# Performance work log

Hardware: AMD Instinct MI355X
Metric: run time of the kernel (lower is better)

## Reference

```python
import jax, jax.numpy as jnp
import numpy as np

NX, NQ, NU, NY = 256, 64, 8, 4
N = 65536
EPS = 0.01
STD = 0.5


def setup_inputs() -> dict:
    key = jax.random.key(0)
    ks = jax.random.split(key, 8)
    return {
        "x": jax.random.normal(ks[0], (N, NX), jnp.float32),
        "u": jax.random.normal(ks[1], (N, NU), jnp.float32),
        "X": jax.random.normal(ks[2], (NX + NQ, NX + NQ), jnp.float32) * STD,
        "U": jax.random.normal(ks[3], (NX, NQ), jnp.float32) * STD,
        "Y1": jax.random.normal(ks[4], (NX, NX), jnp.float32) * STD,
        "XP": jax.random.normal(ks[5], (NX, NX), jnp.float32) * STD,
        "B2": jax.random.normal(ks[6], (NX, NU), jnp.float32) * STD,
        "D12": jax.random.normal(ks[7], (NQ, NU), jnp.float32) * STD,
        "bv": jnp.zeros((NQ,), jnp.float32),
        "t": 0,
    }


def _constrained(X, U, Y1, XP):
    # updateParameters(): build A, B1, C1, D11 from unconstrained params.
    P = XP @ XP.T + EPS * jnp.eye(NX, dtype=XP.dtype)
    H = X @ X.T + EPS * jnp.eye(NX + NQ, dtype=X.dtype)
    H11, H12, H22 = H[:NX, :NX], H[:NX, NX:], H[NX:, NX:]
    Y = -0.5 * (H11 + Y1 - Y1.T)
    Pinv = jnp.linalg.inv(P)
    A = Pinv @ Y                                   # [nx, nx]
    lam = 0.5 * jnp.diagonal(H22)                  # Lambda diagonal
    D11 = -jnp.tril(H22, -1) / lam[:, None]        # strictly lower triangular [nq, nq]
    C1 = U.T / lam[:, None]                        # [nq, nx]
    B1 = Pinv @ (-H12 - U)                         # [nx, nq]
    return A, B1, C1, D11


def _calc_w(base, D11):
    # Forward substitution: w_i = relu(base_i + sum_{j<i} D11[i,j] * w_j).
    # D11 is strictly lower triangular and unfilled w columns are zero, so a
    # full matvec against the carry is exact.
    nq = base.shape[1]

    def step(w, inp):
        i, row, b_col = inp                        # row: [nq], b_col: [Nbatch]
        wi = jax.nn.relu(b_col + w @ row)
        return w.at[:, i].set(wi), None

    w0 = jnp.zeros_like(base)
    w, _ = jax.lax.scan(step, w0, (jnp.arange(nq), D11, base.T))
    return w


def reference(x, u, X, U, Y1, XP, B2, D12, bv, t):
    A, B1, C1, D11 = _constrained(X, U, Y1, XP)
    base = x @ C1.T + u @ D12.T + bv               # [N, nq]
    w = _calc_w(base, D11)
    x_dot = x @ A.T + w @ B1.T + u @ B2.T          # [N, nx]
    return x_dot
```

## Files before the change

kernel.cpp:

```cpp
#include <hip/hip_runtime.h>

#define EPS_C 0.01f

typedef __attribute__((ext_vector_type(8))) short short8;
typedef __attribute__((ext_vector_type(4))) float f32x4;
typedef __attribute__((ext_vector_type(4))) unsigned short u16x4;
typedef __attribute__((ext_vector_type(8))) unsigned short u16x8;

#define WS_H    0
#define WS_C    102400
#define WS_C2   167936
#define WS_Y    233472
#define WS_RHS  299008
#define WS_D11  331776
#define WS_WFH  419840
#define WS_WFM  464896
#define WS_WFL  509952
#define WS_BBH  555008
#define WS_BBM  564224
#define WS_BBL  573440
#define WS_WG   582656
#define WS_E0   4776960
#define WS_E1   4781056

__device__ __forceinline__ int wfoff(int n, int k) {
    return (((n >> 4) * 44 + (k >> 5) * 4 + ((k >> 3) & 3)) << 7) + ((n & 15) << 3) + (k & 7);
}
__device__ __forceinline__ int bboff(int n, int k) {
    return (((n >> 4) * 36 + (k >> 5) * 4 + ((k >> 3) & 3)) << 7) + ((n & 15) << 3) + (k & 7);
}

__device__ __forceinline__ unsigned short f2bf(float f) {
    unsigned int u = __float_as_uint(f);
    unsigned int r = (u + 0x7fffu + ((u >> 16) & 1u)) >> 16;
    return (unsigned short)r;
}
__device__ __forceinline__ float bf2f(unsigned short h) {
    return __uint_as_float(((unsigned int)h) << 16);
}
__device__ __forceinline__ void split1(float f, unsigned short& h, unsigned short& m, unsigned short& l) {
    h = f2bf(f);
    float r1 = f - bf2f(h);
    m = f2bf(r1);
    l = f2bf(r1 - bf2f(m));
}
__device__ __forceinline__ void split8(const float* v, short8& h8, short8& m8, short8& l8) {
#pragma unroll
    for (int j = 0; j < 8; ++j) {
        unsigned short h, m, l;
        split1(v[j], h, m, l);
        h8[j] = (short)h; m8[j] = (short)m; l8[j] = (short)l;
    }
}

__global__ void k_build(const float* __restrict__ Xm, const float* __restrict__ XPm,
                        float* __restrict__ H, float* __restrict__ P) {
    int idx = blockIdx.x * 256 + threadIdx.x;
    if (idx < 102400) {
        int i = idx / 320, j = idx - i * 320;
        const float4* a = (const float4*)(Xm + i * 320);
        const float4* b = (const float4*)(Xm + j * 320);
        float s = 0.f;
        for (int k = 0; k < 80; ++k) {
            float4 va = a[k], vb = b[k];
            s += va.x * vb.x + va.y * vb.y + va.z * vb.z + va.w * vb.w;
        }
        H[idx] = (i == j) ? s + EPS_C : s;
    } else {
        idx -= 102400;
        if (idx < 65536) {
            int i = idx >> 8, j = idx & 255;
            const float4* a = (const float4*)(XPm + i * 256);
            const float4* b = (const float4*)(XPm + j * 256);
            float s = 0.f;
            for (int k = 0; k < 64; ++k) {
                float4 va = a[k], vb = b[k];
                s += va.x * vb.x + va.y * vb.y + va.z * vb.z + va.w * vb.w;
            }
            P[idx] = (i == j) ? s + EPS_C : s;
        }
    }
}

__global__ void k_derived(const float* __restrict__ H, const float* __restrict__ Um,
                          const float* __restrict__ Y1, const float* __restrict__ B2,
                          const float* __restrict__ D12,
                          float* __restrict__ Y, float* __restrict__ RHS,
                          float* __restrict__ D11g,
                          unsigned short* __restrict__ Bh, unsigned short* __restrict__ Bm,
                          unsigned short* __restrict__ Bl,
                          unsigned short* __restrict__ Bbh, unsigned short* __restrict__ Bbm,
                          unsigned short* __restrict__ Bbl) {
    int idx = blockIdx.x * 256 + threadIdx.x;
    if (idx < 65536) {
        int i = idx >> 8, j = idx & 255;
        Y[idx] = -0.5f * (H[i * 320 + j] + Y1[i * 256 + j] - Y1[j * 256 + i]);
        return;
    }
    idx -= 65536;
    if (idx < 16384) {
        RHS[idx] = -H[(idx >> 6) * 320 + 256 + (idx & 63)] - Um[idx];
        return;
    }
    idx -= 16384;
    if (idx < 4096) {
        int q = idx >> 6, j = idx & 63;
        float lam = 0.5f * H[(256 + q) * 320 + 256 + q];
        D11g[idx] = (j < q) ? -H[(256 + q) * 320 + 256 + j] / lam : 0.f;
        return;
    }
    idx -= 4096;
    if (idx < 8192) {
        int o = idx >> 5, cc = idx & 31;
        float f = (cc < 8) ? B2[o * 8 + cc] : 0.f;
        unsigned short h, m, l;
        split1(f, h, m, l);
        int off = wfoff(o, 256 + cc);
        Bh[off] = h; Bm[off] = m; Bl[off] = l;
        return;
    }
    idx -= 8192;
    if (idx < 18432) {
        int q = idx / 288, k = idx - q * 288;
        float f;
        if (k < 256) {
            float lam = 0.5f * H[(256 + q) * 320 + 256 + q];
            f = Um[(size_t)k * 64 + q] / lam;
        } else if (k < 264) f = D12[(size_t)q * 8 + (k - 256)];
        else f = 0.f;
        unsigned short h, m, l;
        split1(f, h, m, l);
        int off = bboff(q, k);
        Bbh[off] = h; Bbm[off] = m; Bbl[off] = l;
    }
}

__global__ void __launch_bounds__(256) k_inv8(const float* __restrict__ Cold, float* __restrict__ E, int b) {
    __shared__ __align__(16) float M[64 * 68];
    __shared__ __align__(16) float Rs[8 * 68];
    __shared__ __align__(16) float Ts[64 * 8];
    __shared__ float E8s[8 * 9];
    const int tid = threadIdx.x;
    const int ti = tid & 15, tj = tid >> 4;
#pragma unroll
    for (int t = 0; t < 4; ++t) {
        int e = tid + t * 256;
        int r = e >> 4, c4 = e & 15;
        float4 v = *(const float4*)&Cold[(size_t)(b * 64 + r) * 256 + b * 64 + c4 * 4];
        *(float4*)&M[r * 68 + c4 * 4] = v;
    }
    __syncthreads();
    for (int s = 0; s < 8; ++s) {
        if (tid < 64) {
            const int lane = tid;
            float e8[8];
#pragma unroll
            for (int j = 0; j < 8; ++j) e8[j] = 0.f;
            if (lane < 8) {
#pragma unroll
                for (int j = 0; j < 8; ++j) e8[j] = M[(s * 8 + lane) * 68 + s * 8 + j];
            }
#pragma unroll
            for (int k = 0; k < 8; ++k) {
                const float p = __shfl(e8[k], k);
                const float rinv = 1.0f / p;
                const float f = -e8[k] * rinv;
                const bool isk = (lane == k);
#pragma unroll
                for (int j = 0; j < 8; ++j) {
                    const float prj = __shfl(e8[j], k);
                    if (j == k) e8[j] = isk ? rinv : f;
                    else        e8[j] = isk ? prj * rinv : fmaf(f, prj, e8[j]);
                }
            }
            if (lane < 8) {
#pragma unroll
                for (int j = 0; j < 8; ++j) E8s[lane * 9 + j] = e8[j];
            }
        }
        __syncthreads();
#pragma unroll
        for (int t = 0; t < 2; ++t) {
            int e = tid + t * 256;
            int r = e >> 6, c = e & 63;
            Rs[r * 68 + c] = M[(s * 8 + r) * 68 + c];
        }
#pragma unroll
        for (int t = 0; t < 2; ++t) {
            int e = tid + t * 256;
            int i = e >> 3, c = e & 7;
            float acc = 0.f;
#pragma unroll
            for (int j = 0; j < 8; ++j) acc = fmaf(M[i * 68 + s * 8 + j], E8s[j * 9 + c], acc);
            Ts[i * 8 + c] = acc;
        }
        __syncthreads();
        {
            const bool rowIn = ((ti >> 1) == s);
            const bool colIn = ((tj >> 1) == s);
            const int i0 = ti * 4, j0 = tj * 4;
            float nv[4][4];
            if (rowIn && colIn) {
#pragma unroll
                for (int r = 0; r < 4; ++r)
#pragma unroll
                    for (int d = 0; d < 4; ++d)
                        nv[r][d] = E8s[(i0 - s * 8 + r) * 9 + (j0 - s * 8 + d)];
            } else if (rowIn) {
#pragma unroll
                for (int r = 0; r < 4; ++r)
#pragma unroll
                    for (int d = 0; d < 4; ++d) {
                        float acc = 0.f;
#pragma unroll
                        for (int c = 0; c < 8; ++c)
                            acc = fmaf(E8s[(i0 - s * 8 + r) * 9 + c], Rs[c * 68 + j0 + d], acc);
                        nv[r][d] = acc;
                    }
            } else if (colIn) {
#pragma unroll
                for (int r = 0; r < 4; ++r)
#pragma unroll
                    for (int d = 0; d < 4; ++d)
                        nv[r][d] = -Ts[(i0 + r) * 8 + (j0 - s * 8 + d)];
            } else {
#pragma unroll
                for (int r = 0; r < 4; ++r)
#pragma unroll
                    for (int d = 0; d < 4; ++d) {
                        float acc = M[(i0 + r) * 68 + j0 + d];
#pragma unroll
                        for (int c = 0; c < 8; ++c)
                            acc = fmaf(-Ts[(i0 + r) * 8 + c], Rs[c * 68 + j0 + d], acc);
                        nv[r][d] = acc;
                    }
            }
#pragma unroll
            for (int r = 0; r < 4; ++r)
#pragma unroll
                for (int d = 0; d < 4; ++d) M[(i0 + r) * 68 + j0 + d] = nv[r][d];
        }
        __syncthreads();
    }
#pragma unroll
    for (int t = 0; t < 4; ++t) {
        int e = tid + t * 256;
        int r = e >> 4, c4 = e & 15;
        float4 v = *(const float4*)&M[r * 68 + c4 * 4];
        *(float4*)&E[(size_t)r * 64 + c4 * 4] = v;
    }
}

__global__ void __launch_bounds__(256) k_gjS(const float* __restrict__ Cold, float* __restrict__ Cnew,
                                             const float* __restrict__ E, float* __restrict__ Eout,
                                             int b, int nb) {
    const int I = blockIdx.x >> 2, J = blockIdx.x & 3;
    const int tid = threadIdx.x;
    const int ti = tid & 15, tj = tid >> 4;
    if (I == b && J == b) {
        const int r = tid >> 2, seg = tid & 3;
#pragma unroll
        for (int t = 0; t < 4; ++t) {
            float4 v = *(const float4*)&E[(size_t)r * 64 + seg * 16 + t * 4];
            *(float4*)&Cnew[(size_t)(b * 64 + r) * 256 + b * 64 + seg * 16 + t * 4] = v;
        }
        return;
    }
    __shared__ __align__(16) float Es[64 * 68];
    __shared__ __align__(16) float S1[64 * 68];
    __shared__ __align__(16) float S2[64 * 68];
    for (int e = tid; e < 1024; e += 256) {
        int r = e >> 4, c4 = e & 15;
        float4 v = *(const float4*)&E[(size_t)r * 64 + c4 * 4];
        *(float4*)&Es[r * 68 + c4 * 4] = v;
    }
    if (I == b) {
        for (int e = tid; e < 1024; e += 256) {
            int r = e >> 4, c4 = e & 15;
            float4 v = *(const float4*)&Cold[(size_t)(b * 64 + r) * 256 + J * 64 + c4 * 4];
            *(float4*)&S1[r * 68 + c4 * 4] = v;
        }
        __syncthreads();
        float acc[4][4];
#pragma unroll
        for (int r = 0; r < 4; ++r)
#pragma unroll
            for (int d = 0; d < 4; ++d) acc[r][d] = 0.f;
        for (int mm = 0; mm < 64; ++mm) {
            float a4[4], b4[4];
#pragma unroll
            for (int d = 0; d < 4; ++d) { a4[d] = Es[(ti * 4 + d) * 68 + mm]; b4[d] = S1[mm * 68 + tj * 4 + d]; }
#pragma unroll
            for (int r = 0; r < 4; ++r)
#pragma unroll
                for (int d = 0; d < 4; ++d) acc[r][d] = fmaf(a4[r], b4[d], acc[r][d]);
        }
#pragma unroll
        for (int r = 0; r < 4; ++r) {
            float4 v = {acc[r][0], acc[r][1], acc[r][2], acc[r][3]};
            *(float4*)&Cnew[(size_t)(b * 64 + ti * 4 + r) * 256 + J * 64 + tj * 4] = v;
        }
        return;
    }
    if (J == b) {
        for (int e = tid; e < 1024; e += 256) {
            int r = e >> 4, c4 = e & 15;
            float4 v = *(const float4*)&Cold[(size_t)(I * 64 + r) * 256 + b * 64 + c4 * 4];
            *(float4*)&S1[r * 68 + c4 * 4] = v;
        }
        __syncthreads();
        float acc[4][4];
#pragma unroll
        for (int r = 0; r < 4; ++r)
#pragma unroll
            for (int d = 0; d < 4; ++d) acc[r][d] = 0.f;
        for (int kk = 0; kk < 64; ++kk) {
            float a4[4], b4[4];
#pragma unroll
            for (int d = 0; d < 4; ++d) { a4[d] = S1[(ti * 4 + d) * 68 + kk]; b4[d] = Es[kk * 68 + tj * 4 + d]; }
#pragma unroll
            for (int r = 0; r < 4; ++r)
#pragma unroll
                for (int d = 0; d < 4; ++d) acc[r][d] = fmaf(a4[r], b4[d], acc[r][d]);
        }
#pragma unroll
        for (int r = 0; r < 4; ++r) {
            float4 v = {-acc[r][0], -acc[r][1], -acc[r][2], -acc[r][3]};
            *(float4*)&Cnew[(size_t)(I * 64 + ti * 4 + r) * 256 + b * 64 + tj * 4] = v;
        }
        return;
    }
    for (int e = tid; e < 1024; e += 256) {
        int r = e >> 4, c4 = e & 15;
        float4 v = *(const float4*)&Cold[(size_t)(I * 64 + r) * 256 + b * 64 + c4 * 4];
        *(float4*)&S1[r * 68 + c4 * 4] = v;
        float4 w = *(const float4*)&Cold[(size_t)(b * 64 + r) * 256 + J * 64 + c4 * 4];
        *(float4*)&S2[r * 68 + c4 * 4] = w;
    }
    __syncthreads();
    float t4[4][4];
#pragma unroll
    for (int r = 0; r < 4; ++r)
#pragma unroll
        for (int d = 0; d < 4; ++d) t4[r][d] = 0.f;
    for (int kk = 0; kk < 64; ++kk) {
        float a4[4], b4[4];
#pragma unroll
        for (int d = 0; d < 4; ++d) { a4[d] = S1[(ti * 4 + d) * 68 + kk]; b4[d] = Es[kk * 68 + tj * 4 + d]; }
#pragma unroll
        for (int r = 0; r < 4; ++r)
#pragma unroll
            for (int d = 0; d < 4; ++d) t4[r][d] = fmaf(a4[r], b4[d], t4[r][d]);
    }
    __syncthreads();
#pragma unroll
    for (int r = 0; r < 4; ++r)
#pragma unroll
        for (int d = 0; d < 4; ++d) S1[(ti * 4 + r) * 68 + tj * 4 + d] = t4[r][d];
    __syncthreads();
    float acc[4][4];
#pragma unroll
    for (int r = 0; r < 4; ++r) {
        float4 cv = *(const float4*)&Cold[(size_t)(I * 64 + ti * 4 + r) * 256 + J * 64 + tj * 4];
        acc[r][0] = cv.x; acc[r][1] = cv.y; acc[r][2] = cv.z; acc[r][3] = cv.w;
    }
    for (int kk = 0; kk < 64; ++kk) {
        float a4[4], b4[4];
#pragma unroll
        for (int d = 0; d < 4; ++d) { a4[d] = S1[(ti * 4 + d) * 68 + kk]; b4[d] = S2[kk * 68 + tj * 4 + d]; }
#pragma unroll
        for (int r = 0; r < 4; ++r)
#pragma unroll
            for (int d = 0; d < 4; ++d) acc[r][d] = fmaf(-a4[r], b4[d], acc[r][d]);
    }
#pragma unroll
    for (int r = 0; r < 4; ++r) {
        float4 v = {acc[r][0], acc[r][1], acc[r][2], acc[r][3]};
        *(float4*)&Cnew[(size_t)(I * 64 + ti * 4 + r) * 256 + J * 64 + tj * 4] = v;
    }
    if (I == nb && J == nb) {
        float* M   = Es;
        float* Rs2 = S2;
        float* Ts2 = S2 + 1024;
        float* E8s = S2 + 1664;
        __syncthreads();
#pragma unroll
        for (int r = 0; r < 4; ++r)
#pragma unroll
            for (int d = 0; d < 4; ++d)
                M[(ti * 4 + r) * 68 + tj * 4 + d] = acc[r][d];
        __syncthreads();
        for (int s = 0; s < 8; ++s) {
            if (tid < 64) {
                const int lane = tid;
                float e8[8];
#pragma unroll
                for (int j = 0; j < 8; ++j) e8[j] = 0.f;
                if (lane < 8) {
#pragma unroll
                    for (int j = 0; j < 8; ++j) e8[j] = M[(s * 8 + lane) * 68 + s * 8 + j];
                }
#pragma unroll
                for (int k = 0; k < 8; ++k) {
                    const float p = __shfl(e8[k], k);
                    const float rinv = 1.0f / p;
                    const float f = -e8[k] * rinv;
                    const bool isk = (lane == k);
#pragma unroll
                    for (int j = 0; j < 8; ++j) {
                        const float prj = __shfl(e8[j], k);
                        if (j == k) e8[j] = isk ? rinv : f;
                        else        e8[j] = isk ? prj * rinv : fmaf(f, prj, e8[j]);
                    }
                }
                if (lane < 8) {
#pragma unroll
                    for (int j = 0; j < 8; ++j) E8s[lane * 9 + j] = e8[j];
                }
            }
            __syncthreads();
#pragma unroll
            for (int t = 0; t < 2; ++t) {
                int e = tid + t * 256;
                int r = e >> 6, c = e & 63;
                Rs2[r * 68 + c] = M[(s * 8 + r) * 68 + c];
            }
#pragma unroll
            for (int t = 0; t < 2; ++t) {
                int e = tid + t * 256;
                int i = e >> 3, c = e & 7;
                float a2 = 0.f;
#pragma unroll
                for (int j = 0; j < 8; ++j) a2 = fmaf(M[i * 68 + s * 8 + j], E8s[j * 9 + c], a2);
                Ts2[i * 8 + c] = a2;
            }
            __syncthreads();
            {
                const bool rowIn = ((ti >> 1) == s);
                const bool colIn = ((tj >> 1) == s);
                const int i0 = ti * 4, j0 = tj * 4;
                float nv[4][4];
                if (rowIn && colIn) {
#pragma unroll
                    for (int r = 0; r < 4; ++r)
#pragma unroll
                        for (int d = 0; d < 4; ++d)
                            nv[r][d] = E8s[(i0 - s * 8 + r) * 9 + (j0 - s * 8 + d)];
                } else if (rowIn) {
#pragma unroll
                    for (int r = 0; r < 4; ++r)
#pragma unroll
                        for (int d = 0; d < 4; ++d) {
                            float a2 = 0.f;
#pragma unroll
                            for (int c = 0; c < 8; ++c)
                                a2 = fmaf(E8s[(i0 - s * 8 + r) * 9 + c], Rs2[c * 68 + j0 + d], a2);
                            nv[r][d] = a2;
                        }
                } else if (colIn) {
#pragma unroll
                    for (int r = 0; r < 4; ++r)
#pragma unroll
                        for (int d = 0; d < 4; ++d)
                            nv[r][d] = -Ts2[(i0 + r) * 8 + (j0 - s * 8 + d)];
                } else {
#pragma unroll
                    for (int r = 0; r < 4; ++r)
#pragma unroll
                        for (int d = 0; d < 4; ++d) {
                            float a2 = M[(i0 + r) * 68 + j0 + d];
#pragma unroll
                            for (int c = 0; c < 8; ++c)
                                a2 = fmaf(-Ts2[(i0 + r) * 8 + c], Rs2[c * 68 + j0 + d], a2);
                            nv[r][d] = a2;
                        }
                }
#pragma unroll
                for (int r = 0; r < 4; ++r)
#pragma unroll
                    for (int d = 0; d < 4; ++d) M[(i0 + r) * 68 + j0 + d] = nv[r][d];
            }
            __syncthreads();
        }
#pragma unroll
        for (int t = 0; t < 4; ++t) {
            int e = tid + t * 256;
            int r = e >> 4, c4 = e & 15;
            float4 v = *(const float4*)&M[r * 68 + c4 * 4];
            *(float4*)&Eout[(size_t)r * 64 + c4 * 4] = v;
        }
    }
}

__global__ void __launch_bounds__(256) k_apply2(const float* __restrict__ PI, const float* __restrict__ Y,
                                                const float* __restrict__ RHS,
                                                unsigned short* __restrict__ Bh, unsigned short* __restrict__ Bm,
                                                unsigned short* __restrict__ Bl) {
    const int i0 = ((int)blockIdx.x / 5) * 64;
    const int c0 = ((int)blockIdx.x % 5) * 64;
    __shared__ __align__(16) float S1[64 * 68], S2[64 * 68];
    const int tid = threadIdx.x;
    const int ti = tid & 15, tj = tid >> 4;
    float acc[4][4];
#pragma unroll
    for (int r = 0; r < 4; ++r)
#pragma unroll
        for (int d = 0; d < 4; ++d) acc[r][d] = 0.f;
    for (int kc = 0; kc < 4; ++kc) {
        __syncthreads();
        for (int e = tid; e < 1024; e += 256) {
            int i = e >> 4, k4 = e & 15;
            float4 v = *(const float4*)&PI[(size_t)(i0 + i) * 256 + kc * 64 + k4 * 4];
            S1[(k4 * 4 + 0) * 68 + i] = v.x;
            S1[(k4 * 4 + 1) * 68 + i] = v.y;
            S1[(k4 * 4 + 2) * 68 + i] = v.z;
            S1[(k4 * 4 + 3) * 68 + i] = v.w;
            float4 w;
            if (c0 < 256) w = *(const float4*)&Y[(size_t)(kc * 64 + i) * 256 + c0 + k4 * 4];
            else          w = *(const float4*)&RHS[(size_t)(kc * 64 + i) * 64 + k4 * 4];
            *(float4*)&S2[i * 68 + k4 * 4] = w;
        }
        __syncthreads();
        for (int kk = 0; kk < 64; ++kk) {
            float4 pv = *(const float4*)&S1[kk * 68 + ti * 4];
            float4 gv = *(const float4*)&S2[kk * 68 + tj * 4];
            float p4[4] = {pv.x, pv.y, pv.z, pv.w};
            float g4[4] = {gv.x, gv.y, gv.z, gv.w};
#pragma unroll
            for (int r = 0; r < 4; ++r)
#pragma unroll
                for (int d = 0; d < 4; ++d) acc[r][d] = fmaf(p4[r], g4[d], acc[r][d]);
        }
    }
    const int pc0 = (c0 < 256) ? c0 : 288;
#pragma unroll
    for (int r = 0; r < 4; ++r)
#pragma unroll
        for (int d = 0; d < 4; ++d) {
            unsigned short h, m, l;
            split1(acc[r][d], h, m, l);
            int off = wfoff(i0 + ti * 4 + r, pc0 + tj * 4 + d);
            Bh[off] = h; Bm[off] = m; Bl[off] = l;
        }
}

#define XSTR 264
__global__ void __launch_bounds__(256, 3) k_base(const float* __restrict__ x, const float* __restrict__ u,
                                                 const unsigned short* __restrict__ Bbh,
                                                 const unsigned short* __restrict__ Bbm,
                                                 const unsigned short* __restrict__ Bbl,
                                                 const float* __restrict__ bv,
                                                 float* __restrict__ wg) {
    __shared__ __align__(16) unsigned short Ah[32 * XSTR];
    __shared__ __align__(16) unsigned short Am[32 * XSTR];
    __shared__ __align__(16) unsigned short Al[32 * XSTR];
    const int tid = threadIdx.x;
    const int r0 = blockIdx.x * 32;
    {
        const float4* xg4 = (const float4*)(x + (size_t)r0 * 256);
#pragma unroll
        for (int i = 0; i < 8; ++i) {
            int e = tid + i * 256, r = e >> 6, c4 = e & 63;
            float4 v = xg4[e];
            float vv[4] = {v.x, v.y, v.z, v.w};
            u16x4 hv, mv, lv;
#pragma unroll
            for (int j = 0; j < 4; ++j) {
                unsigned short h, m, l;
                split1(vv[j], h, m, l);
                hv[j] = h; mv[j] = m; lv[j] = l;
            }
            *(u16x4*)&Ah[r * XSTR + c4 * 4] = hv;
            *(u16x4*)&Am[r * XSTR + c4 * 4] = mv;
            *(u16x4*)&Al[r * XSTR + c4 * 4] = lv;
        }
    }
    __syncthreads();
    const int lane = tid & 63, wid = tid >> 6;
    const int n0 = wid * 16;
    const int lr = lane & 15, lg = lane >> 4;
    const int lk = lg * 8;
    const int fb = wid * 4608 + lg * 128 + lr * 8;
    f32x4 acc[2];
    acc[0] = (f32x4){0.f, 0.f, 0.f, 0.f};
    acc[1] = (f32x4){0.f, 0.f, 0.f, 0.f};
    for (int kt = 0; kt < 9; ++kt) {
        const int ka = kt * 32 + lk;
        short8 a_h[2], a_m[2], a_l[2];
        if (kt < 8) {
            a_h[0] = *(const short8*)&Ah[lr * XSTR + ka];
            a_h[1] = *(const short8*)&Ah[(16 + lr) * XSTR + ka];
            a_m[0] = *(const short8*)&Am[lr * XSTR + ka];
            a_m[1] = *(const short8*)&Am[(16 + lr) * XSTR + ka];
            a_l[0] = *(const short8*)&Al[lr * XSTR + ka];
            a_l[1] = *(const short8*)&Al[(16 + lr) * XSTR + ka];
        } else {
            if (lg == 0) {
                float vv[8];
                const float4* up = (const float4*)&u[(size_t)(r0 + lr) * 8];
                float4 v0 = up[0], v1 = up[1];
                vv[0] = v0.x; vv[1] = v0.y; vv[2] = v0.z; vv[3] = v0.w;
                vv[4] = v1.x; vv[5] = v1.y; vv[6] = v1.z; vv[7] = v1.w;
                split8(vv, a_h[0], a_m[0], a_l[0]);
                const float4* up2 = (const float4*)&u[(size_t)(r0 + 16 + lr) * 8];
                float4 w0 = up2[0], w1 = up2[1];
                vv[0] = w0.x; vv[1] = w0.y; vv[2] = w0.z; vv[3] = w0.w;
                vv[4] = w1.x; vv[5] = w1.y; vv[6] = w1.z; vv[7] = w1.w;
                split8(vv, a_h[1], a_m[1], a_l[1]);
            } else {
                short8 z = {0, 0, 0, 0, 0, 0, 0, 0};
                a_h[0] = z; a_h[1] = z; a_m[0] = z; a_m[1] = z; a_l[0] = z; a_l[1] = z;
            }
        }
        const int off = fb + kt * 512;
        short8 b_h = *(const short8*)&Bbh[off];
        short8 b_m = *(const short8*)&Bbm[off];
        short8 b_l = *(const short8*)&Bbl[off];
#pragma unroll
        for (int m = 0; m < 2; ++m) {
            acc[m] = __builtin_amdgcn_mfma_f32_16x16x32_bf16(a_h[m], b_h, acc[m], 0, 0, 0);
            acc[m] = __builtin_amdgcn_mfma_f32_16x16x32_bf16(a_m[m], b_h, acc[m], 0, 0, 0);
            acc[m] = __builtin_amdgcn_mfma_f32_16x16x32_bf16(a_h[m], b_m, acc[m], 0, 0, 0);
            acc[m] = __builtin_amdgcn_mfma_f32_16x16x32_bf16(a_l[m], b_h, acc[m], 0, 0, 0);
            acc[m] = __builtin_amdgcn_mfma_f32_16x16x32_bf16(a_m[m], b_m, acc[m], 0, 0, 0);
            acc[m] = __builtin_amdgcn_mfma_f32_16x16x32_bf16(a_h[m], b_l, acc[m], 0, 0, 0);
        }
    }
    const float bvv = bv[n0 + lr];
#pragma unroll
    for (int m = 0; m < 2; ++m)
#pragma unroll
        for (int j = 0; j < 4; ++j)
            wg[(size_t)(r0 + m * 16 + lg * 4 + j) * 64 + n0 + lr] = acc[m][j] + bvv;
}

__global__ void __launch_bounds__(256) k_rec(float* __restrict__ wg, const float* __restrict__ D11g) {
    __shared__ float D[64 * 64];
    const int tid = threadIdx.x;
#pragma unroll
    for (int t = 0; t < 16; ++t) D[tid + t * 256] = D11g[tid + t * 256];
    __syncthreads();
    const size_t r = (size_t)blockIdx.x * 256 + tid;
    float w[64];
    float* wr = wg + r * 64;
#pragma unroll
    for (int c = 0; c < 16; ++c) {
        float4 v = *(const float4*)&wr[c * 4];
        w[4 * c] = v.x; w[4 * c + 1] = v.y; w[4 * c + 2] = v.z; w[4 * c + 3] = v.w;
    }
    w[0] = fmaxf(w[0], 0.f);
#pragma unroll
    for (int i = 1; i < 64; ++i) {
        float s0 = w[i], s1 = 0.f, s2 = 0.f, s3 = 0.f;
#pragma unroll
        for (int j = 0; j + 3 < i; j += 4) {
            s0 = fmaf(w[j + 0], D[i * 64 + j + 0], s0);
            s1 = fmaf(w[j + 1], D[i * 64 + j + 1], s1);
            s2 = fmaf(w[j + 2], D[i * 64 + j + 2], s2);
            s3 = fmaf(w[j + 3], D[i * 64 + j + 3], s3);
        }
#pragma unroll
        for (int j = i & ~3; j < i; ++j) s0 = fmaf(w[j], D[i * 64 + j], s0);
        w[i] = fmaxf((s0 + s1) + (s2 + s3), 0.f);
    }
#pragma unroll
    for (int c = 0; c < 16; ++c) {
        float4 v = {w[4 * c], w[4 * c + 1], w[4 * c + 2], w[4 * c + 3]};
        *(float4*)&wr[c * 4] = v;
    }
}

__global__ void __launch_bounds__(256, 3) k_m2(const float* __restrict__ x, const float* __restrict__ wg,
                                               const float* __restrict__ u,
                                               const unsigned short* __restrict__ Bh,
                                               const unsigned short* __restrict__ Bm,
                                               const unsigned short* __restrict__ Bl,
                                               float* __restrict__ out) {
    __shared__ __align__(16) unsigned short Ah[32 * XSTR];
    __shared__ __align__(16) unsigned short Am[32 * XSTR];
    __shared__ __align__(16) unsigned short Al[32 * XSTR];
    const int tid = threadIdx.x;
    const int r0 = blockIdx.x * 32;
    {
        const float4* xg4 = (const float4*)(x + (size_t)r0 * 256);
#pragma unroll
        for (int i = 0; i < 8; ++i) {
            int e = tid + i * 256, r = e >> 6, c4 = e & 63;
            float4 v = xg4[e];
            float vv[4] = {v.x, v.y, v.z, v.w};
            u16x4 hv, mv, lv;
#pragma unroll
            for (int j = 0; j < 4; ++j) {
                unsigned short h, m, l;
                split1(vv[j], h, m, l);
                hv[j] = h; mv[j] = m; lv[j] = l;
            }
            *(u16x4*)&Ah[r * XSTR + c4 * 4] = hv;
            *(u16x4*)&Am[r * XSTR + c4 * 4] = mv;
            *(u16x4*)&Al[r * XSTR + c4 * 4] = lv;
        }
    }
    __syncthreads();
    const int lane = tid & 63, wid = tid >> 6;
    const int n0 = wid * 64;
    const int lr = lane & 15, lg = lane >> 4;
    const int lk = lg * 8;
    const int lgoff = lg * 128 + lr * 8;
    int fb[4];
#pragma unroll
    for (int nf = 0; nf < 4; ++nf) fb[nf] = (wid * 4 + nf) * 5632 + lgoff;
    f32x4 acc[2][4];
#pragma unroll
    for (int m = 0; m < 2; ++m)
#pragma unroll
        for (int nf = 0; nf < 4; ++nf) acc[m][nf] = (f32x4){0.f, 0.f, 0.f, 0.f};

#define M2_MFMA6()                                                                               \
    for (int nf = 0; nf < 4; ++nf) {                                                             \
        for (int m = 0; m < 2; ++m) {                                                            \
            acc[m][nf] = __builtin_amdgcn_mfma_f32_16x16x32_bf16(a_h[m], b_h[nf], acc[m][nf], 0, 0, 0); \
            acc[m][nf] = __builtin_amdgcn_mfma_f32_16x16x32_bf16(a_m[m], b_h[nf], acc[m][nf], 0, 0, 0); \
            acc[m][nf] = __builtin_amdgcn_mfma_f32_16x16x32_bf16(a_h[m], b_m[nf], acc[m][nf], 0, 0, 0); \
            acc[m][nf] = __builtin_amdgcn_mfma_f32_16x16x32_bf16(a_l[m], b_h[nf], acc[m][nf], 0, 0, 0); \
            acc[m][nf] = __builtin_amdgcn_mfma_f32_16x16x32_bf16(a_m[m], b_m[nf], acc[m][nf], 0, 0, 0); \
            acc[m][nf] = __builtin_amdgcn_mfma_f32_16x16x32_bf16(a_h[m], b_l[nf], acc[m][nf], 0, 0, 0); \
        }                                                                                        \
    }

    for (int kt = 0; kt < 8; ++kt) {
        const int ka = kt * 32 + lk;
        short8 a_h[2], a_m[2], a_l[2];
        a_h[0] = *(const short8*)&Ah[lr * XSTR + ka];
        a_h[1] = *(const short8*)&Ah[(16 + lr) * XSTR + ka];
        a_m[0] = *(const short8*)&Am[lr * XSTR + ka];
        a_m[1] = *(const short8*)&Am[(16 + lr) * XSTR + ka];
        a_l[0] = *(const short8*)&Al[lr * XSTR + ka];
        a_l[1] = *(const short8*)&Al[(16 + lr) * XSTR + ka];
        short8 b_h[4], b_m[4], b_l[4];
#pragma unroll
        for (int nf = 0; nf < 4; ++nf) {
            const int off = fb[nf] + kt * 512;
            b_h[nf] = *(const short8*)&Bh[off];
            b_m[nf] = *(const short8*)&Bm[off];
            b_l[nf] = *(const short8*)&Bl[off];
        }
#pragma unroll
        M2_MFMA6()
    }
    {
        short8 a_h[2], a_m[2], a_l[2];
        if (lg == 0) {
            float vv[8];
            const float4* up = (const float4*)&u[(size_t)(r0 + lr) * 8];
            float4 v0 = up[0], v1 = up[1];
            vv[0] = v0.x; vv[1] = v0.y; vv[2] = v0.z; vv[3] = v0.w;
            vv[4] = v1.x; vv[5] = v1.y; vv[6] = v1.z; vv[7] = v1.w;
            split8(vv, a_h[0], a_m[0], a_l[0]);
            const float4* up2 = (const float4*)&u[(size_t)(r0 + 16 + lr) * 8];
            float4 w0 = up2[0], w1 = up2[1];
            vv[0] = w0.x; vv[1] = w0.y; vv[2] = w0.z; vv[3] = w0.w;
            vv[4] = w1.x; vv[5] = w1.y; vv[6] = w1.z; vv[7] = w1.w;
            split8(vv, a_h[1], a_m[1], a_l[1]);
        } else {
            short8 z = {0, 0, 0, 0, 0, 0, 0, 0};
            a_h[0] = z; a_h[1] = z; a_m[0] = z; a_m[1] = z; a_l[0] = z; a_l[1] = z;
        }
        short8 b_h[4], b_m[4], b_l[4];
#pragma unroll
        for (int nf = 0; nf < 4; ++nf) {
            const int off = fb[nf] + 8 * 512;
            b_h[nf] = *(const short8*)&Bh[off];
            b_m[nf] = *(const short8*)&Bm[off];
            b_l[nf] = *(const short8*)&Bl[off];
        }
#pragma unroll
        M2_MFMA6()
    }
    for (int kt = 9; kt < 11; ++kt) {
        const int wc = (kt - 9) * 32 + lk;
        short8 a_h[2], a_m[2], a_l[2];
        {
            float vv[8];
            const float4* wp = (const float4*)&wg[(size_t)(r0 + lr) * 64 + wc];
            float4 v0 = wp[0], v1 = wp[1];
            vv[0] = v0.x; vv[1] = v0.y; vv[2] = v0.z; vv[3] = v0.w;
            vv[4] = v1.x; vv[5] = v1.y; vv[6] = v1.z; vv[7] = v1.w;
            split8(vv, a_h[0], a_m[0], a_l[0]);
            const float4* wp2 = (const float4*)&wg[(size_t)(r0 + 16 + lr) * 64 + wc];
            float4 w0 = wp2[0], w1 = wp2[1];
            vv[0] = w0.x; vv[1] = w0.y; vv[2] = w0.z; vv[3] = w0.w;
            vv[4] = w1.x; vv[5] = w1.y; vv[6] = w1.z; vv[7] = w1.w;
            split8(vv, a_h[1], a_m[1], a_l[1]);
        }
        short8 b_h[4], b_m[4], b_l[4];
#pragma unroll
        for (int nf = 0; nf < 4; ++nf) {
            const int off = fb[nf] + kt * 512;
            b_h[nf] = *(const short8*)&Bh[off];
            b_m[nf] = *(const short8*)&Bm[off];
            b_l[nf] = *(const short8*)&Bl[off];
        }
#pragma unroll
        for (int nf = 0; nf < 4; ++nf) {
#pragma unroll
            for (int m = 0; m < 2; ++m) {
                acc[m][nf] = __builtin_amdgcn_mfma_f32_16x16x32_bf16(a_h[m], b_h[nf], acc[m][nf], 0, 0, 0);
                acc[m][nf] = __builtin_amdgcn_mfma_f32_16x16x32_bf16(a_m[m], b_h[nf], acc[m][nf], 0, 0, 0);
                acc[m][nf] = __builtin_amdgcn_mfma_f32_16x16x32_bf16(a_h[m], b_m[nf], acc[m][nf], 0, 0, 0);
                acc[m][nf] = __builtin_amdgcn_mfma_f32_16x16x32_bf16(a_l[m], b_h[nf], acc[m][nf], 0, 0, 0);
                acc[m][nf] = __builtin_amdgcn_mfma_f32_16x16x32_bf16(a_m[m], b_m[nf], acc[m][nf], 0, 0, 0);
                acc[m][nf] = __builtin_amdgcn_mfma_f32_16x16x32_bf16(a_h[m], b_l[nf], acc[m][nf], 0, 0, 0);
                acc[m][nf] = __builtin_amdgcn_mfma_f32_16x16x32_bf16(a_m[m], b_l[nf], acc[m][nf], 0, 0, 0);
                acc[m][nf] = __builtin_amdgcn_mfma_f32_16x16x32_bf16(a_l[m], b_m[nf], acc[m][nf], 0, 0, 0);
            }
        }
    }
#pragma unroll
    for (int m = 0; m < 2; ++m)
#pragma unroll
        for (int nf = 0; nf < 4; ++nf)
#pragma unroll
            for (int j = 0; j < 4; ++j)
                out[(size_t)(r0 + m * 16 + lg * 4 + j) * 256 + n0 + nf * 16 + lr] = acc[m][nf][j];
}

extern "C" void kernel_launch(void* const* d_in, const int* in_sizes, int n_in,
                              void* d_out, int out_size, void* d_ws, size_t ws_size,
                              hipStream_t stream) {
    const float* x   = (const float*)d_in[0];
    const float* u   = (const float*)d_in[1];
    const float* Xm  = (const float*)d_in[2];
    const float* Um  = (const float*)d_in[3];
    const float* Y1  = (const float*)d_in[4];
    const float* XPm = (const float*)d_in[5];
    const float* B2  = (const float*)d_in[6];
    const float* D12 = (const float*)d_in[7];
    const float* bv  = (const float*)d_in[8];
    float* out = (float*)d_out;
    float* ws  = (float*)d_ws;

    float* H    = ws + WS_H;
    float* C0   = ws + WS_C;
    float* C1   = ws + WS_C2;
    float* Y    = ws + WS_Y;
    float* RHS  = ws + WS_RHS;
    float* D11g = ws + WS_D11;
    float* E0   = ws + WS_E0;
    float* E1   = ws + WS_E1;
    unsigned short* Bh  = (unsigned short*)(ws + WS_WFH);
    unsigned short* Bm  = (unsigned short*)(ws + WS_WFM);
    unsigned short* Bl  = (unsigned short*)(ws + WS_WFL);
    unsigned short* Bbh = (unsigned short*)(ws + WS_BBH);
    unsigned short* Bbm = (unsigned short*)(ws + WS_BBM);
    unsigned short* Bbl = (unsigned short*)(ws + WS_BBL);
    float* wg = ws + WS_WG;

    k_build<<<656, 256, 0, stream>>>(Xm, XPm, H, C0);
    k_derived<<<441, 256, 0, stream>>>(H, Um, Y1, B2, D12, Y, RHS, D11g,
                                       Bh, Bm, Bl, Bbh, Bbm, Bbl);
    k_base<<<2048, 256, 0, stream>>>(x, u, Bbh, Bbm, Bbl, bv, wg);
    k_rec<<<256, 256, 0, stream>>>(wg, D11g);
    k_inv8<<<1, 256, 0, stream>>>(C0, E0, 0);
    k_gjS<<<16, 256, 0, stream>>>(C0, C1, E0, E1, 0, 1);
    k_gjS<<<16, 256, 0, stream>>>(C1, C0, E1, E0, 1, 2);
    k_gjS<<<16, 256, 0, stream>>>(C0, C1, E0, E1, 2, 3);
    k_gjS<<<16, 256, 0, stream>>>(C1, C0, E1, E0, 3, -1);
    k_apply2<<<20, 256, 0, stream>>>(C0, Y, RHS, Bh, Bm, Bl);
    k_m2<<<2048, 256, 0, stream>>>(x, wg, u, Bh, Bm, Bl, out);
}
```

Measured before the change: 340.7 us.

## Fuse matrix inversion stages with grid barrier and merge base with recurrence

Moves the first diagonal-block inverse into an extra block of the derived-parameter kernel. All Gauss-Jordan block steps plus the apply step now run in one persistent kernel that synchronises through an atomic-counter grid barrier, replacing six small launches. The base GEMM and the forward-substitution recurrence are also fused, so w no longer makes a round trip through global memory. The cost is that only 32 threads per block run the recurrence, occupancy drops to 2 blocks per CU, and the spin barrier relies on all 20 blocks being resident at once.

```diff
diff --git a/kernel.cpp b/kernel.cpp
--- a/kernel.cpp
+++ b/kernel.cpp
@@ -22,6 +22,7 @@
 #define WS_WG   582656
 #define WS_E0   4776960
 #define WS_E1   4781056
+#define WS_CTR  4785152
 
 __device__ __forceinline__ int wfoff(int n, int k) {
     return (((n >> 4) * 44 + (k >> 5) * 4 + ((k >> 3) & 3)) << 7) + ((n & 15) << 3) + (k & 7);
@@ -51,6 +52,17 @@
         split1(v[j], h, m, l);
         h8[j] = (short)h; m8[j] = (short)m; l8[j] = (short)l;
     }
+}
+
+__device__ __forceinline__ void gbar(unsigned int* ctr, unsigned int tgt) {
+    __syncthreads();
+    if (threadIdx.x == 0) {
+        __threadfence();
+        atomicAdd(ctr, 1u);
+        while (atomicAdd(ctr, 0u) < tgt) { __builtin_amdgcn_s_sleep(8); }
+        __threadfence();
+    }
+    __syncthreads();
 }
 
 __global__ void k_build(const float* __restrict__ Xm, const float* __restrict__ XPm,
@@ -82,7 +94,7 @@
     }
 }
 
-__global__ void k_derived(const float* __restrict__ H, const float* __restrict__ Um,
+__global__ void __launch_bounds__(256) k_derived(const float* __restrict__ H, const float* __restrict__ Um,
                           const float* __restrict__ Y1, const float* __restrict__ B2,
                           const float* __restrict__ D12,
                           float* __restrict__ Y, float* __restrict__ RHS,
@@ -90,8 +102,126 @@
                           unsigned short* __restrict__ Bh, unsigned short* __restrict__ Bm,
                           unsigned short* __restrict__ Bl,
                           unsigned short* __restrict__ Bbh, unsigned short* __restrict__ Bbm,
-                          unsigned short* __restrict__ Bbl) {
-    int idx = blockIdx.x * 256 + threadIdx.x;
+                          unsigned short* __restrict__ Bbl,
+                          const float* __restrict__ C0, float* __restrict__ E0,
+                          unsigned int* __restrict__ ctr) {
+    __shared__ __align__(16) float M[64 * 68];
+    __shared__ __align__(16) float Rs[8 * 68];
+    __shared__ __align__(16) float Ts[64 * 8];
+    __shared__ float E8s[8 * 9];
+    const int tid = threadIdx.x;
+    if (blockIdx.x == 441) {
+        const int ti = tid & 15, tj = tid >> 4;
+#pragma unroll
+        for (int t = 0; t < 4; ++t) {
+            int e = tid + t * 256;
+            int r = e >> 4, c4 = e & 15;
+            float4 v = *(const float4*)&C0[(size_t)r * 256 + c4 * 4];
+            *(float4*)&M[r * 68 + c4 * 4] = v;
+        }
+        __syncthreads();
+        for (int s = 0; s < 8; ++s) {
+            if (tid < 64) {
+                const int lane = tid;
+                float e8[8];
+#pragma unroll
+                for (int j = 0; j < 8; ++j) e8[j] = 0.f;
+                if (lane < 8) {
+#pragma unroll
+                    for (int j = 0; j < 8; ++j) e8[j] = M[(s * 8 + lane) * 68 + s * 8 + j];
+                }
+#pragma unroll
+                for (int k = 0; k < 8; ++k) {
+                    const float p = __shfl(e8[k], k);
+                    const float rinv = 1.0f / p;
+                    const float f = -e8[k] * rinv;
+                    const bool isk = (lane == k);
+#pragma unroll
+                    for (int j = 0; j < 8; ++j) {
+                        const float prj = __shfl(e8[j], k);
+                        if (j == k) e8[j] = isk ? rinv : f;
+                        else        e8[j] = isk ? prj * rinv : fmaf(f, prj, e8[j]);
+                    }
+                }
+                if (lane < 8) {
+#pragma unroll
+                    for (int j = 0; j < 8; ++j) E8s[lane * 9 + j] = e8[j];
+                }
+            }
+            __syncthreads();
+#pragma unroll
+            for (int t = 0; t < 2; ++t) {
+                int e = tid + t * 256;
+                int r = e >> 6, c = e & 63;
+                Rs[r * 68 + c] = M[(s * 8 + r) * 68 + c];
+            }
+#pragma unroll
+            for (int t = 0; t < 2; ++t) {
+                int e = tid + t * 256;
+                int i = e >> 3, c = e & 7;
+                float acc = 0.f;
+#pragma unroll
+                for (int j = 0; j < 8; ++j) acc = fmaf(M[i * 68 + s * 8 + j], E8s[j * 9 + c], acc);
+                Ts[i * 8 + c] = acc;
+            }
+            __syncthreads();
+            {
+                const bool rowIn = ((ti >> 1) == s);
+                const bool colIn = ((tj >> 1) == s);
+                const int i0 = ti * 4, j0 = tj * 4;
+                float nv[4][4];
+                if (rowIn && colIn) {
+#pragma unroll
+                    for (int r = 0; r < 4; ++r)
+#pragma unroll
+                        for (int d = 0; d < 4; ++d)
+                            nv[r][d] = E8s[(i0 - s * 8 + r) * 9 + (j0 - s * 8 + d)];
+                } else if (rowIn) {
+#pragma unroll
+                    for (int r = 0; r < 4; ++r)
+#pragma unroll
+                        for (int d = 0; d < 4; ++d) {
+                            float acc = 0.f;
+#pragma unroll
+                            for (int c = 0; c < 8; ++c)
+                                acc = fmaf(E8s[(i0 - s * 8 + r) * 9 + c], Rs[c * 68 + j0 + d], acc);
+                            nv[r][d] = acc;
+                        }
+                } else if (colIn) {
+#pragma unroll
+                    for (int r = 0; r < 4; ++r)
+#pragma unroll
+                        for (int d = 0; d < 4; ++d)
+                            nv[r][d] = -Ts[(i0 + r) * 8 + (j0 - s * 8 + d)];
+                } else {
+#pragma unroll
+                    for (int r = 0; r < 4; ++r)
+#pragma unroll
+                        for (int d = 0; d < 4; ++d) {
+                            float acc = M[(i0 + r) * 68 + j0 + d];
+#pragma unroll
+                            for (int c = 0; c < 8; ++c)
+                                acc = fmaf(-Ts[(i0 + r) * 8 + c], Rs[c * 68 + j0 + d], acc);
+                            nv[r][d] = acc;
+                        }
+                }
+#pragma unroll
+                for (int r = 0; r < 4; ++r)
+#pragma unroll
+                    for (int d = 0; d < 4; ++d) M[(i0 + r) * 68 + j0 + d] = nv[r][d];
+            }
+            __syncthreads();
+        }
+#pragma unroll
+        for (int t = 0; t < 4; ++t) {
+            int e = tid + t * 256;
+            int r = e >> 4, c4 = e & 15;
+            float4 v = *(const float4*)&M[r * 68 + c4 * 4];
+            *(float4*)&E0[(size_t)r * 64 + c4 * 4] = v;
+        }
+        return;
+    }
+    int idx = blockIdx.x * 256 + tid;
     if (idx < 65536) {
         int i = idx >> 8, j = idx & 255;
         Y[idx] = -0.5f * (H[i * 320 + j] + Y1[i * 256 + j] - Y1[j * 256 + i]);
@@ -132,428 +262,326 @@
         split1(f, h, m, l);
         int off = bboff(q, k);
         Bbh[off] = h; Bbm[off] = m; Bbl[off] = l;
-    }
-}
-
-__global__ void __launch_bounds__(256) k_inv8(const float* __restrict__ Cold, float* __restrict__ E, int b) {
-    __shared__ __align__(16) float M[64 * 68];
-    __shared__ __align__(16) float Rs[8 * 68];
-    __shared__ __align__(16) float Ts[64 * 8];
-    __shared__ float E8s[8 * 9];
-    const int tid = threadIdx.x;
-    const int ti = tid & 15, tj = tid >> 4;
-#pragma unroll
-    for (int t = 0; t < 4; ++t) {
-        int e = tid + t * 256;
-        int r = e >> 4, c4 = e & 15;
-        float4 v = *(const float4*)&Cold[(size_t)(b * 64 + r) * 256 + b * 64 + c4 * 4];
-        *(float4*)&M[r * 68 + c4 * 4] = v;
-    }
-    __syncthreads();
-    for (int s = 0; s < 8; ++s) {
-        if (tid < 64) {
-            const int lane = tid;
-            float e8[8];
-#pragma unroll
-            for (int j = 0; j < 8; ++j) e8[j] = 0.f;
-            if (lane < 8) {
-#pragma unroll
-                for (int j = 0; j < 8; ++j) e8[j] = M[(s * 8 + lane) * 68 + s * 8 + j];
-            }
-#pragma unroll
-            for (int k = 0; k < 8; ++k) {
-                const float p = __shfl(e8[k], k);
-                const float rinv = 1.0f / p;
-                const float f = -e8[k] * rinv;
-                const bool isk = (lane == k);
-#pragma unroll
-                for (int j = 0; j < 8; ++j) {
-                    const float prj = __shfl(e8[j], k);
-                    if (j == k) e8[j] = isk ? rinv : f;
-                    else        e8[j] = isk ? prj * rinv : fmaf(f, prj, e8[j]);
-                }
-            }
-            if (lane < 8) {
-#pragma unroll
-                for (int j = 0; j < 8; ++j) E8s[lane * 9 + j] = e8[j];
-            }
-        }
-        __syncthreads();
-#pragma unroll
-        for (int t = 0; t < 2; ++t) {
-            int e = tid + t * 256;
-            int r = e >> 6, c = e & 63;
-            Rs[r * 68 + c] = M[(s * 8 + r) * 68 + c];
-        }
-#pragma unroll
-        for (int t = 0; t < 2; ++t) {
-            int e = tid + t * 256;
-            int i = e >> 3, c = e & 7;
-            float acc = 0.f;
-#pragma unroll
-            for (int j = 0; j < 8; ++j) acc = fmaf(M[i * 68 + s * 8 + j], E8s[j * 9 + c], acc);
-            Ts[i * 8 + c] = acc;
-        }
-        __syncthreads();
-        {
-            const bool rowIn = ((ti >> 1) == s);
-            const bool colIn = ((tj >> 1) == s);
-            const int i0 = ti * 4, j0 = tj * 4;
-            float nv[4][4];
-            if (rowIn && colIn) {
-#pragma unroll
-                for (int r = 0; r < 4; ++r)
-#pragma unroll
-                    for (int d = 0; d < 4; ++d)
-                        nv[r][d] = E8s[(i0 - s * 8 + r) * 9 + (j0 - s * 8 + d)];
-            } else if (rowIn) {
-#pragma unroll
-                for (int r = 0; r < 4; ++r)
-#pragma unroll
-                    for (int d = 0; d < 4; ++d) {
-                        float acc = 0.f;
-#pragma unroll
-                        for (int c = 0; c < 8; ++c)
-                            acc = fmaf(E8s[(i0 - s * 8 + r) * 9 + c], Rs[c * 68 + j0 + d], acc);
-                        nv[r][d] = acc;
-                    }
-            } else if (colIn) {
-#pragma unroll
-                for (int r = 0; r < 4; ++r)
-#pragma unroll
-                    for (int d = 0; d < 4; ++d)
-                        nv[r][d] = -Ts[(i0 + r) * 8 + (j0 - s * 8 + d)];
-            } else {
-#pragma unroll
-                for (int r = 0; r < 4; ++r)
-#pragma unroll
-                    for (int d = 0; d < 4; ++d) {
-                        float acc = M[(i0 + r) * 68 + j0 + d];
-#pragma unroll
-                        for (int c = 0; c < 8; ++c)
-                            acc = fmaf(-Ts[(i0 + r) * 8 + c], Rs[c * 68 + j0 + d], acc);
-                        nv[r][d] = acc;
-                    }
-            }
-#pragma unroll
-            for (int r = 0; r < 4; ++r)
-#pragma unroll
-                for (int d = 0; d < 4; ++d) M[(i0 + r) * 68 + j0 + d] = nv[r][d];
-        }
-        __syncthreads();
-    }
-#pragma unroll
-    for (int t = 0; t < 4; ++t) {
-        int e = tid + t * 256;
-        int r = e >> 4, c4 = e & 15;
-        float4 v = *(const float4*)&M[r * 68 + c4 * 4];
-        *(float4*)&E[(size_t)r * 64 + c4 * 4] = v;
-    }
-}
-
-__global__ void __launch_bounds__(256) k_gjS(const float* __restrict__ Cold, float* __restrict__ Cnew,
-                                             const float* __restrict__ E, float* __restrict__ Eout,
-                                             int b, int nb) {
-    const int I = blockIdx.x >> 2, J = blockIdx.x & 3;
-    const int tid = threadIdx.x;
-    const int ti = tid & 15, tj = tid >> 4;
-    if (I == b && J == b) {
-        const int r = tid >> 2, seg = tid & 3;
-#pragma unroll
-        for (int t = 0; t < 4; ++t) {
-            float4 v = *(const float4*)&E[(size_t)r * 64 + seg * 16 + t * 4];
-            *(float4*)&Cnew[(size_t)(b * 64 + r) * 256 + b * 64 + seg * 16 + t * 4] = v;
-        }
         return;
     }
+    idx -= 18432;
+    if (idx == 0) *ctr = 0u;
+}
+
+__global__ void __launch_bounds__(256) k_gjall(float* __restrict__ C0, float* __restrict__ C1,
+                                               float* __restrict__ E0, float* __restrict__ E1,
+                                               const float* __restrict__ Y, const float* __restrict__ RHS,
+                                               unsigned short* __restrict__ Bh, unsigned short* __restrict__ Bm,
+                                               unsigned short* __restrict__ Bl,
+                                               unsigned int* __restrict__ ctr) {
     __shared__ __align__(16) float Es[64 * 68];
     __shared__ __align__(16) float S1[64 * 68];
     __shared__ __align__(16) float S2[64 * 68];
-    for (int e = tid; e < 1024; e += 256) {
-        int r = e >> 4, c4 = e & 15;
-        float4 v = *(const float4*)&E[(size_t)r * 64 + c4 * 4];
-        *(float4*)&Es[r * 68 + c4 * 4] = v;
-    }
-    if (I == b) {
-        for (int e = tid; e < 1024; e += 256) {
-            int r = e >> 4, c4 = e & 15;
-            float4 v = *(const float4*)&Cold[(size_t)(b * 64 + r) * 256 + J * 64 + c4 * 4];
-            *(float4*)&S1[r * 68 + c4 * 4] = v;
-        }
-        __syncthreads();
+    const int tid = threadIdx.x;
+    const int bid = blockIdx.x;
+    const int ti = tid & 15, tj = tid >> 4;
+    unsigned int ph = 0;
+    for (int b = 0; b < 4; ++b) {
+        const float* Cold = (b & 1) ? C1 : C0;
+        float* Cnew = (b & 1) ? C0 : C1;
+        const float* E = (b & 1) ? E1 : E0;
+        float* Eout = (b & 1) ? E0 : E1;
+        const int nb = b + 1;
+        if (bid < 16) {
+            const int I = bid >> 2, J = bid & 3;
+            if (I == b && J == b) {
+                const int r = tid >> 2, seg = tid & 3;
+#pragma unroll
+                for (int t = 0; t < 4; ++t) {
+                    float4 v = *(const float4*)&E[(size_t)r * 64 + seg * 16 + t * 4];
+                    *(float4*)&Cnew[(size_t)(b * 64 + r) * 256 + b * 64 + seg * 16 + t * 4] = v;
+                }
+            } else {
+                for (int e = tid; e < 1024; e += 256) {
+                    int r = e >> 4, c4 = e & 15;
+                    float4 v = *(const float4*)&E[(size_t)r * 64 + c4 * 4];
+                    *(float4*)&Es[r * 68 + c4 * 4] = v;
+                }
+                if (I == b) {
+                    for (int e = tid; e < 1024; e += 256) {
+                        int r = e >> 4, c4 = e & 15;
+                        float4 v = *(const float4*)&Cold[(size_t)(b * 64 + r) * 256 + J * 64 + c4 * 4];
+                        *(float4*)&S1[r * 68 + c4 * 4] = v;
+                    }
+                    __syncthreads();
+                    float acc[4][4];
+#pragma unroll
+                    for (int r = 0; r < 4; ++r)
+#pragma unroll
+                        for (int d = 0; d < 4; ++d) acc[r][d] = 0.f;
+                    for (int mm = 0; mm < 64; ++mm) {
+                        float a4[4], b4[4];
+#pragma unroll
+                        for (int d = 0; d < 4; ++d) { a4[d] = Es[(ti * 4 + d) * 68 + mm]; b4[d] = S1[mm * 68 + tj * 4 + d]; }
+#pragma unroll
+                        for (int r = 0; r < 4; ++r)
+#pragma unroll
+                            for (int d = 0; d < 4; ++d) acc[r][d] = fmaf(a4[r], b4[d], acc[r][d]);
+                    }
+#pragma unroll
+                    for (int r = 0; r < 4; ++r) {
+                        float4 v = {acc[r][0], acc[r][1], acc[r][2], acc[r][3]};
+                        *(float4*)&Cnew[(size_t)(b * 64 + ti * 4 + r) * 256 + J * 64 + tj * 4] = v;
+                    }
+                    __syncthreads();
+                } else if (J == b) {
+                    for (int e = tid; e < 1024; e += 256) {
+                        int r = e >> 4, c4 = e & 15;
+                        float4 v = *(const float4*)&Cold[(size_t)(I * 64 + r) * 256 + b * 64 + c4 * 4];
+                        *(float4*)&S1[r * 68 + c4 * 4] = v;
+                    }
+                    __syncthreads();
+                    float acc[4][4];
+#pragma unroll
+                    for (int r = 0; r < 4; ++r)
+#pragma unroll
+                        for (int d = 0; d < 4; ++d) acc[r][d] = 0.f;
+                    for (int kk = 0; kk < 64; ++kk) {
+                        float a4[4], b4[4];
+#pragma unroll
+                        for (int d = 0; d < 4; ++d) { a4[d] = S1[(ti * 4 + d) * 68 + kk]; b4[d] = Es[kk * 68 + tj * 4 + d]; }
+#pragma unroll
+                        for (int r = 0; r < 4; ++r)
+#pragma unroll
+                            for (int d = 0; d < 4; ++d) acc[r][d] = fmaf(a4[r], b4[d], acc[r][d]);
+                    }
+#pragma unroll
+                    for (int r = 0; r < 4; ++r) {
+                        float4 v = {-acc[r][0], -acc[r][1], -acc[r][2], -acc[r][3]};
+                        *(float4*)&Cnew[(size_t)(I * 64 + ti * 4 + r) * 256 + b * 64 + tj * 4] = v;
+                    }
+                    __syncthreads();
+                } else {
+                    for (int e = tid; e < 1024; e += 256) {
+                        int r = e >> 4, c4 = e & 15;
+                        float4 v = *(const float4*)&Cold[(size_t)(I * 64 + r) * 256 + b * 64 + c4 * 4];
+                        *(float4*)&S1[r * 68 + c4 * 4] = v;
+                        float4 w = *(const float4*)&Cold[(size_t)(b * 64 + r) * 256 + J * 64 + c4 * 4];
+                        *(float4*)&S2[r * 68 + c4 * 4] = w;
+                    }
+                    __syncthreads();
+                    float t4[4][4];
+#pragma unroll
+                    for (int r = 0; r < 4; ++r)
+#pragma unroll
+                        for (int d = 0; d < 4; ++d) t4[r][d] = 0.f;
+                    for (int kk = 0; kk < 64; ++kk) {
+                        float a4[4], b4[4];
+#pragma unroll
+                        for (int d = 0; d < 4; ++d) { a4[d] = S1[(ti * 4 + d) * 68 + kk]; b4[d] = Es[kk * 68 + tj * 4 + d]; }
+#pragma unroll
+                        for (int r = 0; r < 4; ++r)
+#pragma unroll
+                            for (int d = 0; d < 4; ++d) t4[r][d] = fmaf(a4[r], b4[d], t4[r][d]);
+                    }
+                    __syncthreads();
+#pragma unroll
+                    for (int r = 0; r < 4; ++r)
+#pragma unroll
+                        for (int d = 0; d < 4; ++d) S1[(ti * 4 + r) * 68 + tj * 4 + d] = t4[r][d];
+                    __syncthreads();
+                    float acc[4][4];
+#pragma unroll
+                    for (int r = 0; r < 4; ++r) {
+                        float4 cv = *(const float4*)&Cold[(size_t)(I * 64 + ti * 4 + r) * 256 + J * 64 + tj * 4];
+                        acc[r][0] = cv.x; acc[r][1] = cv.y; acc[r][2] = cv.z; acc[r][3] = cv.w;
+                    }
+                    for (int kk = 0; kk < 64; ++kk) {
+                        float a4[4], b4[4];
+#pragma unroll
+                        for (int d = 0; d < 4; ++d) { a4[d] = S1[(ti * 4 + d) * 68 + kk]; b4[d] = S2[kk * 68 + tj * 4 + d]; }
+#pragma unroll
+                        for (int r = 0; r < 4; ++r)
+#pragma unroll
+                            for (int d = 0; d < 4; ++d) acc[r][d] = fmaf(-a4[r], b4[d], acc[r][d]);
+                    }
+#pragma unroll
+                    for (int r = 0; r < 4; ++r) {
+                        float4 v = {acc[r][0], acc[r][1], acc[r][2], acc[r][3]};
+                        *(float4*)&Cnew[(size_t)(I * 64 + ti * 4 + r) * 256 + J * 64 + tj * 4] = v;
+                    }
+                    if (I == nb && J == nb) {
+                        float* M   = Es;
+                        float* Rs2 = S2;
+                        float* Ts2 = S2 + 1024;
+                        float* E8s = S2 + 1664;
+                        __syncthreads();
+#pragma unroll
+                        for (int r = 0; r < 4; ++r)
+#pragma unroll
+                            for (int d = 0; d < 4; ++d)
+                                M[(ti * 4 + r) * 68 + tj * 4 + d] = acc[r][d];
+                        __syncthreads();
+                        for (int s = 0; s < 8; ++s) {
+                            if (tid < 64) {
+                                const int lane = tid;
+                                float e8[8];
+#pragma unroll
+                                for (int j = 0; j < 8; ++j) e8[j] = 0.f;
+                                if (lane < 8) {
+#pragma unroll
+                                    for (int j = 0; j < 8; ++j) e8[j] = M[(s * 8 + lane) * 68 + s * 8 + j];
+                                }
+#pragma unroll
+                                for (int k = 0; k < 8; ++k) {
+                                    const float p = __shfl(e8[k], k);
+                                    const float rinv = 1.0f / p;
+                                    const float f = -e8[k] * rinv;
+                                    const bool isk = (lane == k);
+#pragma unroll
+                                    for (int j = 0; j < 8; ++j) {
+                                        const float prj = __shfl(e8[j], k);
+                                        if (j == k) e8[j] = isk ? rinv : f;
+                                        else        e8[j] = isk ? prj * rinv : fmaf(f, prj, e8[j]);
+                                    }
+                                }
+                                if (lane < 8) {
+#pragma unroll
+                                    for (int j = 0; j < 8; ++j) E8s[lane * 9 + j] = e8[j];
+                                }
+                            }
+                            __syncthreads();
+#pragma unroll
+                            for (int t = 0; t < 2; ++t) {
+                                int e = tid + t * 256;
+                                int r = e >> 6, c = e & 63;
+                                Rs2[r * 68 + c] = M[(s * 8 + r) * 68 + c];
+                            }
+#pragma unroll
+                            for (int t = 0; t < 2; ++t) {
+                                int e = tid + t * 256;
+                                int i = e >> 3, c = e & 7;
+                                float a2 = 0.f;
+#pragma unroll
+                                for (int j = 0; j < 8; ++j) a2 = fmaf(M[i * 68 + s * 8 + j], E8s[j * 9 + c], a2);
+                                Ts2[i * 8 + c] = a2;
+                            }
+                            __syncthreads();
+                            {
+                                const bool rowIn = ((ti >> 1) == s);
+                                const bool colIn = ((tj >> 1) == s);
+                                const int i0 = ti * 4, j0 = tj * 4;
+                                float nv[4][4];
+                                if (rowIn && colIn) {
+#pragma unroll
+                                    for (int r = 0; r < 4; ++r)
+#pragma unroll
+                                        for (int d = 0; d < 4; ++d)
+                                            nv[r][d] = E8s[(i0 - s * 8 + r) * 9 + (j0 - s * 8 + d)];
+                                } else if (rowIn) {
+#pragma unroll
+                                    for (int r = 0; r < 4; ++r)
+#pragma unroll
+                                        for (int d = 0; d < 4; ++d) {
+                                            float a2 = 0.f;
+#pragma unroll
+                                            for (int c = 0; c < 8; ++c)
+                                                a2 = fmaf(E8s[(i0 - s * 8 + r) * 9 + c], Rs2[c * 68 + j0 + d], a2);
+                                            nv[r][d] = a2;
+                                        }
+                                } else if (colIn) {
+#pragma unroll
+                                    for (int r = 0; r < 4; ++r)
+#pragma unroll
+                                        for (int d = 0; d < 4; ++d)
+                                            nv[r][d] = -Ts2[(i0 + r) * 8 + (j0 - s * 8 + d)];
+                                } else {
+#pragma unroll
+                                    for (int r = 0; r < 4; ++r)
+#pragma unroll
+                                        for (int d = 0; d < 4; ++d) {
+                                            float a2 = M[(i0 + r) * 68 + j0 + d];
+#pragma unroll
+                                            for (int c = 0; c < 8; ++c)
+                                                a2 = fmaf(-Ts2[(i0 + r) * 8 + c], Rs2[c * 68 + j0 + d], a2);
+                                            nv[r][d] = a2;
+                                        }
+                                }
+#pragma unroll
+                                for (int r = 0; r < 4; ++r)
+#pragma unroll
+                                    for (int d = 0; d < 4; ++d) M[(i0 + r) * 68 + j0 + d] = nv[r][d];
+                            }
+                            __syncthreads();
+                        }
+#pragma unroll
+                        for (int t = 0; t < 4; ++t) {
+                            int e = tid + t * 256;
+                            int r = e >> 4, c4 = e & 15;
+                            float4 v = *(const float4*)&M[r * 68 + c4 * 4];
+                            *(float4*)&Eout[(size_t)r * 64 + c4 * 4] = v;
+                        }
+                    }
+                }
+            }
+        }
+        gbar(ctr, 20u * ++ph);
+    }
+    {
+        const int i0 = (bid / 5) * 64;
+        const int c0 = (bid % 5) * 64;
         float acc[4][4];
 #pragma unroll
         for (int r = 0; r < 4; ++r)
 #pragma unroll
             for (int d = 0; d < 4; ++d) acc[r][d] = 0.f;
-        for (int mm = 0; mm < 64; ++mm) {
-            float a4[4], b4[4];
-#pragma unroll
-            for (int d = 0; d < 4; ++d) { a4[d] = Es[(ti * 4 + d) * 68 + mm]; b4[d] = S1[mm * 68 + tj * 4 + d]; }
-#pragma unroll
-            for (int r = 0; r < 4; ++r)
-#pragma unroll
-                for (int d = 0; d < 4; ++d) acc[r][d] = fmaf(a4[r], b4[d], acc[r][d]);
-        }
-#pragma unroll
-        for (int r = 0; r < 4; ++r) {
-            float4 v = {acc[r][0], acc[r][1], acc[r][2], acc[r][3]};
-            *(float4*)&Cnew[(size_t)(b * 64 + ti * 4 + r) * 256 + J * 64 + tj * 4] = v;
-        }
-        return;
-    }
-    if (J == b) {
-        for (int e = tid; e < 1024; e += 256) {
-            int r = e >> 4, c4 = e & 15;
-            float4 v = *(const float4*)&Cold[(size_t)(I * 64 + r) * 256 + b * 64 + c4 * 4];
-            *(float4*)&S1[r * 68 + c4 * 4] = v;
-        }
-        __syncthreads();
-        float acc[4][4];
+        for (int kc = 0; kc < 4; ++kc) {
+            __syncthreads();
+            for (int e = tid; e < 1024; e += 256) {
+                int i = e >> 4, k4 = e & 15;
+                float4 v = *(const float4*)&C0[(size_t)(i0 + i) * 256 + kc * 64 + k4 * 4];
+                S1[(k4 * 4 + 0) * 68 + i] = v.x;
+                S1[(k4 * 4 + 1) * 68 + i] = v.y;
+                S1[(k4 * 4 + 2) * 68 + i] = v.z;
+                S1[(k4 * 4 + 3) * 68 + i] = v.w;
+                float4 w;
+                if (c0 < 256) w = *(const float4*)&Y[(size_t)(kc * 64 + i) * 256 + c0 + k4 * 4];
+                else          w = *(const float4*)&RHS[(size_t)(kc * 64 + i) * 64 + k4 * 4];
+                *(float4*)&S2[i * 68 + k4 * 4] = w;
+            }
+            __syncthreads();
+            for (int kk = 0; kk < 64; ++kk) {
+                float4 pv = *(const float4*)&S1[kk * 68 + ti * 4];
+                float4 gv = *(const float4*)&S2[kk * 68 + tj * 4];
+                float p4[4] = {pv.x, pv.y, pv.z, pv.w};
+                float g4[4] = {gv.x, gv.y, gv.z, gv.w};
+#pragma unroll
+                for (int r = 0; r < 4; ++r)
+#pragma unroll
+                    for (int d = 0; d < 4; ++d) acc[r][d] = fmaf(p4[r], g4[d], acc[r][d]);
+            }
+        }
+        const int pc0 = (c0 < 256) ? c0 : 288;
 #pragma unroll
         for (int r = 0; r < 4; ++r)
 #pragma unroll
-            for (int d = 0; d < 4; ++d) acc[r][d] = 0.f;
-        for (int kk = 0; kk < 64; ++kk) {
-            float a4[4], b4[4];
-#pragma unroll
-            for (int d = 0; d < 4; ++d) { a4[d] = S1[(ti * 4 + d) * 68 + kk]; b4[d] = Es[kk * 68 + tj * 4 + d]; }
-#pragma unroll
-            for (int r = 0; r < 4; ++r)
-#pragma unroll
-                for (int d = 0; d < 4; ++d) acc[r][d] = fmaf(a4[r], b4[d], acc[r][d]);
-        }
-#pragma unroll
-        for (int r = 0; r < 4; ++r) {
-            float4 v = {-acc[r][0], -acc[r][1], -acc[r][2], -acc[r][3]};
-            *(float4*)&Cnew[(size_t)(I * 64 + ti * 4 + r) * 256 + b * 64 + tj * 4] = v;
-        }
-        return;
-    }
-    for (int e = tid; e < 1024; e += 256) {
-        int r = e >> 4, c4 = e & 15;
-        float4 v = *(const float4*)&Cold[(size_t)(I * 64 + r) * 256 + b * 64 + c4 * 4];
-        *(float4*)&S1[r * 68 + c4 * 4] = v;
-        float4 w = *(const float4*)&Cold[(size_t)(b * 64 + r) * 256 + J * 64 + c4 * 4];
-        *(float4*)&S2[r * 68 + c4 * 4] = w;
-    }
-    __syncthreads();
-    float t4[4][4];
-#pragma unroll
-    for (int r = 0; r < 4; ++r)
-#pragma unroll
-        for (int d = 0; d < 4; ++d) t4[r][d] = 0.f;
-    for (int kk = 0; kk < 64; ++kk) {
-        float a4[4], b4[4];
-#pragma unroll
-        for (int d = 0; d < 4; ++d) { a4[d] = S1[(ti * 4 + d) * 68 + kk]; b4[d] = Es[kk * 68 + tj * 4 + d]; }
-#pragma unroll
-        for (int r = 0; r < 4; ++r)
-#pragma unroll
-            for (int d = 0; d < 4; ++d) t4[r][d] = fmaf(a4[r], b4[d], t4[r][d]);
-    }
-    __syncthreads();
-#pragma unroll
-    for (int r = 0; r < 4; ++r)
-#pragma unroll
-        for (int d = 0; d < 4; ++d) S1[(ti * 4 + r) * 68 + tj * 4 + d] = t4[r][d];
-    __syncthreads();
-    float acc[4][4];
-#pragma unroll
-    for (int r = 0; r < 4; ++r) {
-        float4 cv = *(const float4*)&Cold[(size_t)(I * 64 + ti * 4 + r) * 256 + J * 64 + tj * 4];
-        acc[r][0] = cv.x; acc[r][1] = cv.y; acc[r][2] = cv.z; acc[r][3] = cv.w;
-    }
-    for (int kk = 0; kk < 64; ++kk) {
-        float a4[4], b4[4];
-#pragma unroll
-        for (int d = 0; d < 4; ++d) { a4[d] = S1[(ti * 4 + d) * 68 + kk]; b4[d] = S2[kk * 68 + tj * 4 + d]; }
-#pragma unroll
-        for (int r = 0; r < 4; ++r)
-#pragma unroll
-            for (int d = 0; d < 4; ++d) acc[r][d] = fmaf(-a4[r], b4[d], acc[r][d]);
-    }
-#pragma unroll
-    for (int r = 0; r < 4; ++r) {
-        float4 v = {acc[r][0], acc[r][1], acc[r][2], acc[r][3]};
-        *(float4*)&Cnew[(size_t)(I * 64 + ti * 4 + r) * 256 + J * 64 + tj * 4] = v;
-    }
-    if (I == nb && J == nb) {
-        float* M   = Es;
-        float* Rs2 = S2;
-        float* Ts2 = S2 + 1024;
-        float* E8s = S2 + 1664;
-        __syncthreads();
-#pragma unroll
-        for (int r = 0; r < 4; ++r)
-#pragma unroll
-            for (int d = 0; d < 4; ++d)
-                M[(ti * 4 + r) * 68 + tj * 4 + d] = acc[r][d];
-        __syncthreads();
-        for (int s = 0; s < 8; ++s) {
-            if (tid < 64) {
-                const int lane = tid;
-                float e8[8];
-#pragma unroll
-                for (int j = 0; j < 8; ++j) e8[j] = 0.f;
-                if (lane < 8) {
-#pragma unroll
-                    for (int j = 0; j < 8; ++j) e8[j] = M[(s * 8 + lane) * 68 + s * 8 + j];
-                }
-#pragma unroll
-                for (int k = 0; k < 8; ++k) {
-                    const float p = __shfl(e8[k], k);
-                    const float rinv = 1.0f / p;
-                    const float f = -e8[k] * rinv;
-                    const bool isk = (lane == k);
-#pragma unroll
-                    for (int j = 0; j < 8; ++j) {
-                        const float prj = __shfl(e8[j], k);
-                        if (j == k) e8[j] = isk ? rinv : f;
-                        else        e8[j] = isk ? prj * rinv : fmaf(f, prj, e8[j]);
-                    }
-                }
-                if (lane < 8) {
-#pragma unroll
-                    for (int j = 0; j < 8; ++j) E8s[lane * 9 + j] = e8[j];
-                }
-            }
-            __syncthreads();
-#pragma unroll
-            for (int t = 0; t < 2; ++t) {
-                int e = tid + t * 256;
-                int r = e >> 6, c = e & 63;
-                Rs2[r * 68 + c] = M[(s * 8 + r) * 68 + c];
-            }
-#pragma unroll
-            for (int t = 0; t < 2; ++t) {
-                int e = tid + t * 256;
-                int i = e >> 3, c = e & 7;
-                float a2 = 0.f;
-#pragma unroll
-                for (int j = 0; j < 8; ++j) a2 = fmaf(M[i * 68 + s * 8 + j], E8s[j * 9 + c], a2);
-                Ts2[i * 8 + c] = a2;
-            }
-            __syncthreads();
-            {
-                const bool rowIn = ((ti >> 1) == s);
-                const bool colIn = ((tj >> 1) == s);
-                const int i0 = ti * 4, j0 = tj * 4;
-                float nv[4][4];
-                if (rowIn && colIn) {
-#pragma unroll
-                    for (int r = 0; r < 4; ++r)
-#pragma unroll
-                        for (int d = 0; d < 4; ++d)
-                            nv[r][d] = E8s[(i0 - s * 8 + r) * 9 + (j0 - s * 8 + d)];
-                } else if (rowIn) {
-#pragma unroll
-                    for (int r = 0; r < 4; ++r)
-#pragma unroll
-                        for (int d = 0; d < 4; ++d) {
-                            float a2 = 0.f;
-#pragma unroll
-                            for (int c = 0; c < 8; ++c)
-                                a2 = fmaf(E8s[(i0 - s * 8 + r) * 9 + c], Rs2[c * 68 + j0 + d], a2);
-                            nv[r][d] = a2;
-                        }
-                } else if (colIn) {
-#pragma unroll
-                    for (int r = 0; r < 4; ++r)
-#pragma unroll
-                        for (int d = 0; d < 4; ++d)
-                            nv[r][d] = -Ts2[(i0 + r) * 8 + (j0 - s * 8 + d)];
-                } else {
-#pragma unroll
-                    for (int r = 0; r < 4; ++r)
-#pragma unroll
-                        for (int d = 0; d < 4; ++d) {
-                            float a2 = M[(i0 + r) * 68 + j0 + d];
-#pragma unroll
-                            for (int c = 0; c < 8; ++c)
-                                a2 = fmaf(-Ts2[(i0 + r) * 8 + c], Rs2[c * 68 + j0 + d], a2);
-                            nv[r][d] = a2;
-                        }
-                }
-#pragma unroll
-                for (int r = 0; r < 4; ++r)
-#pragma unroll
-                    for (int d = 0; d < 4; ++d) M[(i0 + r) * 68 + j0 + d] = nv[r][d];
-            }
-            __syncthreads();
-        }
-#pragma unroll
-        for (int t = 0; t < 4; ++t) {
-            int e = tid + t * 256;
-            int r = e >> 4, c4 = e & 15;
-            float4 v = *(const float4*)&M[r * 68 + c4 * 4];
-            *(float4*)&Eout[(size_t)r * 64 + c4 * 4] = v;
-        }
-    }
-}
-
-__global__ void __launch_bounds__(256) k_apply2(const float* __restrict__ PI, const float* __restrict__ Y,
-                                                const float* __restrict__ RHS,
-                                                unsigned short* __restrict__ Bh, unsigned short* __restrict__ Bm,
-                                                unsigned short* __restrict__ Bl) {
-    const int i0 = ((int)blockIdx.x / 5) * 64;
-    const int c0 = ((int)blockIdx.x % 5) * 64;
-    __shared__ __align__(16) float S1[64 * 68], S2[64 * 68];
-    const int tid = threadIdx.x;
-    const int ti = tid & 15, tj = tid >> 4;
-    float acc[4][4];
-#pragma unroll
-    for (int r = 0; r < 4; ++r)
-#pragma unroll
-        for (int d = 0; d < 4; ++d) acc[r][d] = 0.f;
-    for (int kc = 0; kc < 4; ++kc) {
-        __syncthreads();
-        for (int e = tid; e < 1024; e += 256) {
-            int i = e >> 4, k4 = e & 15;
-            float4 v = *(const float4*)&PI[(size_t)(i0 + i) * 256 + kc * 64 + k4 * 4];
-            S1[(k4 * 4 + 0) * 68 + i] = v.x;
-            S1[(k4 * 4 + 1) * 68 + i] = v.y;
-            S1[(k4 * 4 + 2) * 68 + i] = v.z;
-            S1[(k4 * 4 + 3) * 68 + i] = v.w;
-            float4 w;
-            if (c0 < 256) w = *(const float4*)&Y[(size_t)(kc * 64 + i) * 256 + c0 + k4 * 4];
-            else          w = *(const float4*)&RHS[(size_t)(kc * 64 + i) * 64 + k4 * 4];
-            *(float4*)&S2[i * 68 + k4 * 4] = w;
-        }
-        __syncthreads();
-        for (int kk = 0; kk < 64; ++kk) {
-            float4 pv = *(const float4*)&S1[kk * 68 + ti * 4];
-            float4 gv = *(const float4*)&S2[kk * 68 + tj * 4];
-            float p4[4] = {pv.x, pv.y, pv.z, pv.w};
-            float g4[4] = {gv.x, gv.y, gv.z, gv.w};
-#pragma unroll
-            for (int r = 0; r < 4; ++r)
-#pragma unroll
-                for (int d = 0; d < 4; ++d) acc[r][d] = fmaf(p4[r], g4[d], acc[r][d]);
-        }
-    }
-    const int pc0 = (c0 < 256) ? c0 : 288;
-#pragma unroll
-    for (int r = 0; r < 4; ++r)
-#pragma unroll
-        for (int d = 0; d < 4; ++d) {
-            unsigned short h, m, l;
-            split1(acc[r][d], h, m, l);
-            int off = wfoff(i0 + ti * 4 + r, pc0 + tj * 4 + d);
-            Bh[off] = h; Bm[off] = m; Bl[off] = l;
-        }
+            for (int d = 0; d < 4; ++d) {
+                unsigned short h, m, l;
+                split1(acc[r][d], h, m, l);
+                int off = wfoff(i0 + ti * 4 + r, pc0 + tj * 4 + d);
+                Bh[off] = h; Bm[off] = m; Bl[off] = l;
+            }
+    }
 }
 
 #define XSTR 264
-__global__ void __launch_bounds__(256, 3) k_base(const float* __restrict__ x, const float* __restrict__ u,
-                                                 const unsigned short* __restrict__ Bbh,
-                                                 const unsigned short* __restrict__ Bbm,
-                                                 const unsigned short* __restrict__ Bbl,
-                                                 const float* __restrict__ bv,
-                                                 float* __restrict__ wg) {
+__global__ void __launch_bounds__(256, 2) k_basrec(const float* __restrict__ x, const float* __restrict__ u,
+                                                   const unsigned short* __restrict__ Bbh,
+                                                   const unsigned short* __restrict__ Bbm,
+                                                   const unsigned short* __restrict__ Bbl,
+                                                   const float* __restrict__ bv,
+                                                   const float* __restrict__ D11g,
+                                                   float* __restrict__ wg) {
     __shared__ __align__(16) unsigned short Ah[32 * XSTR];
     __shared__ __align__(16) unsigned short Am[32 * XSTR];
     __shared__ __align__(16) unsigned short Al[32 * XSTR];
+    __shared__ float bs[32 * 65];
+    __shared__ float Ds[64 * 64];
     const int tid = threadIdx.x;
     const int r0 = blockIdx.x * 32;
     {
@@ -574,6 +602,8 @@
             *(u16x4*)&Am[r * XSTR + c4 * 4] = mv;
             *(u16x4*)&Al[r * XSTR + c4 * 4] = lv;
         }
+#pragma unroll
+        for (int t = 0; t < 16; ++t) Ds[tid + t * 256] = D11g[tid + t * 256];
     }
     __syncthreads();
     const int lane = tid & 63, wid = tid >> 6;
@@ -626,47 +656,40 @@
             acc[m] = __builtin_amdgcn_mfma_f32_16x16x32_bf16(a_h[m], b_l, acc[m], 0, 0, 0);
         }
     }
-    const float bvv = bv[n0 + lr];
-#pragma unroll
-    for (int m = 0; m < 2; ++m)
-#pragma unroll
-        for (int j = 0; j < 4; ++j)
-            wg[(size_t)(r0 + m * 16 + lg * 4 + j) * 64 + n0 + lr] = acc[m][j] + bvv;
-}
-
-__global__ void __launch_bounds__(256) k_rec(float* __restrict__ wg, const float* __restrict__ D11g) {
-    __shared__ float D[64 * 64];
-    const int tid = threadIdx.x;
-#pragma unroll
-    for (int t = 0; t < 16; ++t) D[tid + t * 256] = D11g[tid + t * 256];
+    {
+        const float bvv = bv[n0 + lr];
+#pragma unroll
+        for (int m = 0; m < 2; ++m)
+#pragma unroll
+            for (int j = 0; j < 4; ++j)
+                bs[(m * 16 + lg * 4 + j) * 65 + n0 + lr] = acc[m][j] + bvv;
+    }
     __syncthreads();
-    const size_t r = (size_t)blockIdx.x * 256 + tid;
-    float w[64];
-    float* wr = wg + r * 64;
-#pragma unroll
-    for (int c = 0; c < 16; ++c) {
-        float4 v = *(const float4*)&wr[c * 4];
-        w[4 * c] = v.x; w[4 * c + 1] = v.y; w[4 * c + 2] = v.z; w[4 * c + 3] = v.w;
-    }
-    w[0] = fmaxf(w[0], 0.f);
-#pragma unroll
-    for (int i = 1; i < 64; ++i) {
-        float s0 = w[i], s1 = 0.f, s2 = 0.f, s3 = 0.f;
-#pragma unroll
-        for (int j = 0; j + 3 < i; j += 4) {
-            s0 = fmaf(w[j + 0], D[i * 64 + j + 0], s0);
-            s1 = fmaf(w[j + 1], D[i * 64 + j + 1], s1);
-            s2 = fmaf(w[j + 2], D[i * 64 + j + 2], s2);
-            s3 = fmaf(w[j + 3], D[i * 64 + j + 3], s3);
-        }
-#pragma unroll
-        for (int j = i & ~3; j < i; ++j) s0 = fmaf(w[j], D[i * 64 + j], s0);
-        w[i] = fmaxf((s0 + s1) + (s2 + s3), 0.f);
-    }
-#pragma unroll
-    for (int c = 0; c < 16; ++c) {
-        float4 v = {w[4 * c], w[4 * c + 1], w[4 * c + 2], w[4 * c + 3]};
-        *(float4*)&wr[c * 4] = v;
+    if (tid < 32) {
+        float w[64];
+#pragma unroll
+        for (int c = 0; c < 64; ++c) w[c] = bs[tid * 65 + c];
+        w[0] = fmaxf(w[0], 0.f);
+#pragma unroll
+        for (int i = 1; i < 64; ++i) {
+            float s0 = w[i], s1 = 0.f, s2 = 0.f, s3 = 0.f;
+#pragma unroll
+            for (int j = 0; j + 3 < i; j += 4) {
+                s0 = fmaf(w[j + 0], Ds[i * 64 + j + 0], s0);
+                s1 = fmaf(w[j + 1], Ds[i * 64 + j + 1], s1);
+                s2 = fmaf(w[j + 2], Ds[i * 64 + j + 2], s2);
+                s3 = fmaf(w[j + 3], Ds[i * 64 + j + 3], s3);
+            }
+#pragma unroll
+            for (int j = i & ~3; j < i; ++j) s0 = fmaf(w[j], Ds[i * 64 + j], s0);
+            w[i] = fmaxf((s0 + s1) + (s2 + s3), 0.f);
+        }
+        float* wr = wg + (size_t)(r0 + tid) * 64;
+#pragma unroll
+        for (int c = 0; c < 16; ++c) {
+            float4 v = {w[4 * c], w[4 * c + 1], w[4 * c + 2], w[4 * c + 3]};
+            *(float4*)&wr[c * 4] = v;
+        }
     }
 }
 
@@ -847,6 +870,7 @@
     float* D11g = ws + WS_D11;
     float* E0   = ws + WS_E0;
     float* E1   = ws + WS_E1;
+    unsigned int* ctr = (unsigned int*)(ws + WS_CTR);
     unsigned short* Bh  = (unsigned short*)(ws + WS_WFH);
     unsigned short* Bm  = (unsigned short*)(ws + WS_WFM);
     unsigned short* Bl  = (unsigned short*)(ws + WS_WFL);
@@ -856,15 +880,9 @@
     float* wg = ws + WS_WG;
 
     k_build<<<656, 256, 0, stream>>>(Xm, XPm, H, C0);
-    k_derived<<<441, 256, 0, stream>>>(H, Um, Y1, B2, D12, Y, RHS, D11g,
-                                       Bh, Bm, Bl, Bbh, Bbm, Bbl);
-    k_base<<<2048, 256, 0, stream>>>(x, u, Bbh, Bbm, Bbl, bv, wg);
-    k_rec<<<256, 256, 0, stream>>>(wg, D11g);
-    k_inv8<<<1, 256, 0, stream>>>(C0, E0, 0);
-    k_gjS<<<16, 256, 0, stream>>>(C0, C1, E0, E1, 0, 1);
-    k_gjS<<<16, 256, 0, stream>>>(C1, C0, E1, E0, 1, 2);
-    k_gjS<<<16, 256, 0, stream>>>(C0, C1, E0, E1, 2, 3);
-    k_gjS<<<16, 256, 0, stream>>>(C1, C0, E1, E0, 3, -1);
-    k_apply2<<<20, 256, 0, stream>>>(C0, Y, RHS, Bh, Bm, Bl);
+    k_derived<<<442, 256, 0, stream>>>(H, Um, Y1, B2, D12, Y, RHS, D11g,
+                                       Bh, Bm, Bl, Bbh, Bbm, Bbl, C0, E0, ctr);
+    k_gjall<<<20, 256, 0, stream>>>(C0, C1, E0, E1, Y, RHS, Bh, Bm, Bl, ctr);
+    k_basrec<<<2048, 256, 0, stream>>>(x, u, Bbh, Bbm, Bbl, bv, D11g, wg);
     k_m2<<<2048, 256, 0, stream>>>(x, wg, u, Bh, Bm, Bl, out);
 }
```

After: 358.4 us. 5.2% more time.
